# Optimization experiments

Hardware: AMD Instinct MI355X
Metric: run time of the kernel (lower is better)

## Reference

```python
import jax, jax.numpy as jnp
import numpy as np

H = 512  # hidden_size


def setup_inputs() -> dict:
    key = jax.random.key(0)
    ks = jax.random.split(key, 8)
    B, L = 16, 2048
    query = jax.random.normal(ks[0], (B, 1, 2 * H), dtype=jnp.float32)
    keys = jax.random.normal(ks[1], (B, L, 2 * H), dtype=jnp.float32)
    coverage = jax.random.uniform(ks[2], (B, L, 1), dtype=jnp.float32)
    # alignment MLP: Linear(4H+1 -> 2H, bias) -> tanh -> Linear(2H -> 1, no bias) -> softmax(dim=1)
    s1 = 1.0 / np.sqrt(4 * H + 1)
    W1 = jax.random.uniform(ks[3], (4 * H + 1, 2 * H), jnp.float32, -s1, s1)
    b1 = jax.random.uniform(ks[4], (2 * H,), jnp.float32, -s1, s1)
    s2 = 1.0 / np.sqrt(2 * H)
    W2 = jax.random.uniform(ks[5], (2 * H, 1), jnp.float32, -s2, s2)
    # reduce: Linear(2H -> H, no bias)
    Wr = jax.random.uniform(ks[6], (2 * H, H), jnp.float32, -s2, s2)
    return {"query": query, "keys": keys, "coverage": coverage,
            "W1": W1, "b1": b1, "W2": W2, "Wr": Wr}


def reference(query, keys, coverage, W1, b1, W2, Wr):
    B, L, _ = keys.shape
    q = jnp.broadcast_to(query, (B, L, query.shape[-1]))          # (B,L,2H)
    feat = jnp.concatenate([q, keys, coverage], axis=-1)          # (B,L,4H+1)
    h = jnp.tanh(feat @ W1 + b1)                                  # (B,L,2H)
    scores = h @ W2                                               # (B,L,1)
    attention = jax.nn.softmax(scores, axis=1)                    # softmax over length
    reduced = keys @ Wr                                           # (B,L,H)
    context = jnp.einsum('blo,blh->boh', attention, reduced)      # (B,1,H)
    return context, attention
```

## Files before the change

kernel.cpp:

```cpp
#include <hip/hip_runtime.h>
#include <hip/hip_bf16.h>
#include <stdint.h>

typedef short bf16x8 __attribute__((ext_vector_type(8)));
typedef float f32x4 __attribute__((ext_vector_type(4)));
typedef unsigned int u32x2 __attribute__((ext_vector_type(2)));
typedef unsigned int u32x4 __attribute__((ext_vector_type(4)));

__device__ __forceinline__ uint32_t pack2f(float lo, float hi) {
  union { __hip_bfloat162 h; uint32_t u; } c;
  c.h.x = __float2bfloat16(lo);
  c.h.y = __float2bfloat16(hi);
  return c.u;
}

__device__ __forceinline__ unsigned short f32_to_bf16(float f) {
  union { __hip_bfloat16 h; unsigned short u; } c;
  c.h = __float2bfloat16(f);
  return c.u;
}

__device__ __forceinline__ float bfbits_to_f32(uint32_t hi16) {
  union { uint32_t u; float f; } c;
  c.u = hi16 << 16;
  return c.f;
}

__device__ __forceinline__ float fast_tanh(float x) {
  float e = __builtin_amdgcn_exp2f(x * 2.8853900817779268f);
  return 1.0f - 2.0f * __builtin_amdgcn_rcpf(e + 1.0f);
}

#define GLD16(g, l)                                                                    \
  __builtin_amdgcn_global_load_lds((const __attribute__((address_space(1))) void*)(g), \
                                   (__attribute__((address_space(3))) void*)(l), 16, 0, 0)

#define MFMA16(a, b, c) __builtin_amdgcn_mfma_f32_16x16x32_bf16(a, b, c, 0, 0, 0)
#define SBAR0() __builtin_amdgcn_sched_barrier(0)

__global__ void transpose_w1k(const float* __restrict__ W1, unsigned short* __restrict__ W1kt) {
  __shared__ float t[64][65];
  const int kb = blockIdx.x * 64;
  const int jb = blockIdx.y * 64;
  const int c = threadIdx.x & 63;
  const int r = threadIdx.x >> 6;
#pragma unroll
  for (int i = 0; i < 16; ++i) {
    const int k = i * 4 + r;
    t[k][c] = W1[(size_t)(1024 + kb + k) * 1024 + (jb + c)];
  }
  __syncthreads();
#pragma unroll
  for (int i = 0; i < 16; ++i) {
    const int j = i * 4 + r;
    W1kt[(size_t)(jb + j) * 1024 + (kb + c)] = f32_to_bf16(t[c][j]);
  }
}

__global__ void convert_keys(const float* __restrict__ keys, unsigned short* __restrict__ keysbf) {
  const int bid = blockIdx.x, tid = threadIdx.x;
#pragma unroll
  for (int it = 0; it < 2; ++it) {
    const size_t c8 = ((size_t)bid * 512 + it * 256 + tid) * 8;
    f32x4 a = *(const f32x4*)(keys + c8);
    f32x4 b = *(const f32x4*)(keys + c8 + 4);
    u32x4 p;
    p.x = pack2f(a.x, a.y);
    p.y = pack2f(a.z, a.w);
    p.z = pack2f(b.x, b.y);
    p.w = pack2f(b.z, b.w);
    *(u32x4*)(keysbf + c8) = p;
  }
}

__global__ void qterm_kernel(const float* __restrict__ query, const float* __restrict__ W1,
                             const float* __restrict__ b1, float* __restrict__ qterm) {
  const int b = blockIdx.y;
  const int j = blockIdx.x * 64 + (threadIdx.x & 63);
  const int kq = threadIdx.x >> 6;
  __shared__ float part[4][64];
  const float* q = query + b * 1024 + kq * 256;
  const float* wp = W1 + (size_t)(kq * 256) * 1024 + j;
  float acc = 0.f;
#pragma unroll 8
  for (int k = 0; k < 256; ++k) acc += q[k] * wp[(size_t)k * 1024];
  part[kq][threadIdx.x & 63] = acc;
  __syncthreads();
  if (threadIdx.x < 64) {
    const int jj = blockIdx.x * 64 + threadIdx.x;
    qterm[b * 1024 + jj] = b1[jj] + part[0][threadIdx.x] + part[1][threadIdx.x] +
                           part[2][threadIdx.x] + part[3][threadIdx.x];
  }
}


#define STAGE_T(t_, src, Dd)                               \
  _Pragma("unroll") for (int i = 0; i < 4; ++i) {          \
    const int r = w * 32 + i * 8 + (lane >> 3);            \
    const int u = (lane & 7) ^ (r & 7);                    \
    GLD16((src) + (((size_t)r) << 10) + (t_) * 64 + u * 8, \
          (Dd) + w * 4096 + lane * 16 + i * 1024);         \
  }

#define V11_COMPUTE(Asrc, Bsrc)                                                          \
  _Pragma("unroll") for (int kk = 0; kk < 2; ++kk) {                                     \
    bf16x8 af[8], bfv[4];                                                                \
    _Pragma("unroll") for (int mf = 0; mf < 8; ++mf) {                                   \
      const int ra = wm * 128 + mf * 16 + c16;                                           \
      af[mf] = *(const bf16x8*)((Asrc) + ra * 128 + (((kk * 4 + q4) ^ (ra & 7)) << 4));  \
    }                                                                                    \
    _Pragma("unroll") for (int nf = 0; nf < 4; ++nf) {                                   \
      const int ca = wn * 64 + nf * 16 + c16;                                            \
      bfv[nf] = *(const bf16x8*)((Bsrc) + ca * 128 + (((kk * 4 + q4) ^ (ca & 7)) << 4)); \
    }                                                                                    \
    _Pragma("unroll") for (int nf = 0; nf < 4; ++nf)                                     \
        _Pragma("unroll") for (int mf = 0; mf < 8; ++mf) acc[mf][nf] =                   \
            MFMA16(af[mf], bfv[nf], acc[mf][nf]);                                        \
  }

#define V11_ITER(t_, Ac, Bc, An, Bn)                          \
  if ((t_) < 15) {                                            \
    STAGE_T((t_) + 1, gAbase, An);                            \
    STAGE_T((t_) + 1, gBbase, Bn);                            \
  }                                                           \
  SBAR0();                                                    \
  V11_COMPUTE(Ac, Bc);                                        \
  SBAR0();                                                    \
  asm volatile("s_waitcnt vmcnt(0) lgkmcnt(0)" ::: "memory"); \
  __builtin_amdgcn_s_barrier();

__global__ __launch_bounds__(512, 2) void gemm_score_v11(
    const unsigned short* __restrict__ keysbf, const unsigned short* __restrict__ W1kt,
    const float* __restrict__ qterm, const float* __restrict__ coverage,
    const float* __restrict__ W1, const float* __restrict__ W2,
    float* __restrict__ scores_part) {
  __shared__ __align__(16) unsigned char lds[135168];
  unsigned char* A0 = lds;
  unsigned char* A1 = lds + 32768;
  unsigned char* B0 = lds + 65536;
  unsigned char* B1 = lds + 98304;
  float* Sred = (float*)(lds + 131072);

  const int tid = threadIdx.x;
  const int bid = blockIdx.x;
  const int xcd = bid & 7;
  const int idx = bid >> 3;
  const int rowt = xcd * 16 + (idx >> 2);
  const int colgrp = idx & 3;
  const int row0 = rowt * 256;
  const int col0 = colgrp * 256;
  const int b = row0 >> 11;
  const int w = tid >> 6;
  const int wm = w >> 2, wn = w & 3;
  const int lane = tid & 63;
  const int c16 = lane & 15, q4 = lane >> 4;

  const unsigned short* gAbase = keysbf + ((size_t)row0 << 10);
  const unsigned short* gBbase = W1kt + ((size_t)col0 << 10);

  f32x4 acc[8][4];
  const f32x4 zz = {0.f, 0.f, 0.f, 0.f};
#pragma unroll
  for (int mf = 0; mf < 8; ++mf)
#pragma unroll
    for (int nf = 0; nf < 4; ++nf) acc[mf][nf] = zz;

  STAGE_T(0, gAbase, A0);
  STAGE_T(0, gBbase, B0);
  asm volatile("s_waitcnt vmcnt(0)" ::: "memory");
  __builtin_amdgcn_s_barrier();

#pragma unroll 1
  for (int th = 0; th < 8; ++th) {
    const int t0 = th * 2, t1 = th * 2 + 1;
    V11_ITER(t0, A0, B0, A1, B1);
    V11_ITER(t1, A1, B1, A0, B0);
  }

  float covv[8][4];
#pragma unroll
  for (int mf = 0; mf < 8; ++mf)
#pragma unroll
    for (int r = 0; r < 4; ++r)
      covv[mf][r] = coverage[row0 + wm * 128 + mf * 16 + q4 * 4 + r];

  float p_part[8][4];
#pragma unroll
  for (int mf = 0; mf < 8; ++mf)
#pragma unroll
    for (int r = 0; r < 4; ++r) p_part[mf][r] = 0.f;

#pragma unroll
  for (int nf = 0; nf < 4; ++nf) {
    const int col = col0 + wn * 64 + nf * 16 + c16;
    const float qt = qterm[b * 1024 + col];
    const float w1c = W1[(size_t)2048 * 1024 + col];
    const float w2 = W2[col];
#pragma unroll
    for (int mf = 0; mf < 8; ++mf)
#pragma unroll
      for (int r = 0; r < 4; ++r) {
        float v = acc[mf][nf][r] + qt + covv[mf][r] * w1c;
        p_part[mf][r] += fast_tanh(v) * w2;
      }
  }

#pragma unroll
  for (int mf = 0; mf < 8; ++mf)
#pragma unroll
    for (int r = 0; r < 4; ++r) {
      float p = p_part[mf][r];
      p += __shfl_xor(p, 1);
      p += __shfl_xor(p, 2);
      p += __shfl_xor(p, 4);
      p += __shfl_xor(p, 8);
      if (c16 == 0) Sred[w * 128 + mf * 16 + q4 * 4 + r] = p;
    }
  __syncthreads();
  if (tid < 256) {
    const int wmv = tid >> 7, rl = tid & 127;
    float s = Sred[(wmv * 4 + 0) * 128 + rl] + Sred[(wmv * 4 + 1) * 128 + rl] +
              Sred[(wmv * 4 + 2) * 128 + rl] + Sred[(wmv * 4 + 3) * 128 + rl];
    scores_part[(size_t)colgrp * 32768 + row0 + tid] = s;
  }
}

__global__ void softmax_kernel(const float* __restrict__ sp, float* __restrict__ att) {
  const int b = blockIdx.x;
  const int tid = threadIdx.x;
  float* a = att + b * 2048;
  __shared__ float red[4];
  float mx = -1e30f;
  for (int l = tid; l < 2048; l += 256) {
    float v = 0.f;
#pragma unroll
    for (int g = 0; g < 4; ++g) v += sp[(size_t)g * 32768 + b * 2048 + l];
    a[l] = v;
    mx = fmaxf(mx, v);
  }
#pragma unroll
  for (int o = 1; o < 64; o <<= 1) mx = fmaxf(mx, __shfl_xor(mx, o));
  if ((tid & 63) == 0) red[tid >> 6] = mx;
  __syncthreads();
  mx = fmaxf(fmaxf(red[0], red[1]), fmaxf(red[2], red[3]));
  __syncthreads();
  float sum = 0.f;
  for (int l = tid; l < 2048; l += 256) {
    float e = __expf(a[l] - mx);
    a[l] = e;
    sum += e;
  }
#pragma unroll
  for (int o = 1; o < 64; o <<= 1) sum += __shfl_xor(sum, o);
  if ((tid & 63) == 0) red[tid >> 6] = sum;
  __syncthreads();
  sum = red[0] + red[1] + red[2] + red[3];
  const float inv = 1.0f / sum;
  for (int l = tid; l < 2048; l += 256) a[l] *= inv;
}

__global__ void ctxpre_kernel(const unsigned short* __restrict__ keysbf,
                              const float* __restrict__ att, float* __restrict__ ctx_part) {
  const int b = blockIdx.x;
  const int sl = blockIdx.y;
  const int tid = threadIdx.x;
  const float* ab = att + b * 2048 + sl * 128;
  const unsigned short* kb = keysbf + ((size_t)b * 2048 + sl * 128) * 1024 + tid * 4;
  f32x4 acc = {0.f, 0.f, 0.f, 0.f};
#pragma unroll 4
  for (int l = 0; l < 128; ++l) {
    u32x2 v = *(const u32x2*)(kb + (size_t)l * 1024);
    const float al = ab[l];
    acc.x += bfbits_to_f32(v.x & 0xFFFFu) * al;
    acc.y += bfbits_to_f32(v.x >> 16) * al;
    acc.z += bfbits_to_f32(v.y & 0xFFFFu) * al;
    acc.w += bfbits_to_f32(v.y >> 16) * al;
  }
  *(f32x4*)(ctx_part + ((size_t)(sl * 16 + b)) * 1024 + tid * 4) = acc;
}

__global__ void ctxreduce_kernel(const float* __restrict__ ctx_part, float* __restrict__ ctx_pre) {
  const int i = blockIdx.x * 256 + threadIdx.x;
  const int b = i >> 10, j = i & 1023;
  float s = 0.f;
#pragma unroll
  for (int sl = 0; sl < 16; ++sl) s += ctx_part[((size_t)(sl * 16 + b)) * 1024 + j];
  ctx_pre[i] = s;
}

__global__ void context_kernel(const float* __restrict__ ctx_pre, const float* __restrict__ Wr,
                               float* __restrict__ out) {
  const int b = blockIdx.y;
  const int h = blockIdx.x * 64 + (threadIdx.x & 63);
  const int jq = threadIdx.x >> 6;
  __shared__ float part[4][64];
  const float* cp = ctx_pre + b * 1024 + jq * 256;
  const float* wp = Wr + (size_t)(jq * 256) * 512 + h;
  float acc = 0.f;
#pragma unroll 8
  for (int k = 0; k < 256; ++k) acc += cp[k] * wp[(size_t)k * 512];
  part[jq][threadIdx.x & 63] = acc;
  __syncthreads();
  if (threadIdx.x < 64)
    out[b * 512 + blockIdx.x * 64 + threadIdx.x] = part[0][threadIdx.x] + part[1][threadIdx.x] +
                                                   part[2][threadIdx.x] + part[3][threadIdx.x];
}

extern "C" void kernel_launch(void* const* d_in, const int* in_sizes, int n_in, void* d_out,
                              int out_size, void* d_ws, size_t ws_size, hipStream_t stream) {
  const float* query = (const float*)d_in[0];
  const float* keys = (const float*)d_in[1];
  const float* coverage = (const float*)d_in[2];
  const float* W1 = (const float*)d_in[3];
  const float* b1 = (const float*)d_in[4];
  const float* W2 = (const float*)d_in[5];
  const float* Wr = (const float*)d_in[6];
  float* out = (float*)d_out;
  char* ws = (char*)d_ws;

  float* scores_part = (float*)ws;
  float* ctx_part = (float*)ws;
  float* ctx_pre = (float*)(ws + 1048576);
  float* qterm = (float*)(ws + 1114112);
  unsigned short* W1kt = (unsigned short*)(ws + 1179648);
  unsigned short* keysbf = (unsigned short*)(ws + 3276800);

  float* context_out = out;
  float* att_out = out + 8192;

  transpose_w1k<<<dim3(16, 16), dim3(256), 0, stream>>>(W1, W1kt);
  convert_keys<<<dim3(8192), dim3(256), 0, stream>>>(keys, keysbf);
  qterm_kernel<<<dim3(16, 16), dim3(256), 0, stream>>>(query, W1, b1, qterm);
  gemm_score_v11<<<dim3(512), dim3(512), 0, stream>>>(keysbf, W1kt, qterm, coverage, W1, W2,
                                                      scores_part);
  softmax_kernel<<<dim3(16), dim3(256), 0, stream>>>(scores_part, att_out);
  ctxpre_kernel<<<dim3(16, 16), dim3(256), 0, stream>>>(keysbf, att_out, ctx_part);
  ctxreduce_kernel<<<dim3(64), dim3(256), 0, stream>>>(ctx_part, ctx_pre);
  context_kernel<<<dim3(8, 16), dim3(256), 0, stream>>>(ctx_pre, Wr, context_out);
}
```

Before: 164.0 us.

## Triple-buffer GEMM K-loop and merge prep and context kernels

Replaces the double-buffered K=64 GEMM main loop with a three-stage K=32 pipeline. It waits with a partial vmcnt so that loads stay in flight across the barrier, and raises wave priority around the MFMA block. The three preprocessing kernels (key conversion, W1 transpose, qterm) are merged into one launch, and the ctx reduce is fused into the final context projection, cutting launches. The cost is a smaller k-step, more barriers per tile, and redundant reduction of ctx_part across the 8 hb blocks.

Result: faster. 147.0 us (-10.4%).

```diff
diff --git a/kernel.cpp b/kernel.cpp
--- a/kernel.cpp
+++ b/kernel.cpp
@@ -38,108 +38,111 @@
 #define MFMA16(a, b, c) __builtin_amdgcn_mfma_f32_16x16x32_bf16(a, b, c, 0, 0, 0)
 #define SBAR0() __builtin_amdgcn_sched_barrier(0)
 
-__global__ void transpose_w1k(const float* __restrict__ W1, unsigned short* __restrict__ W1kt) {
-  __shared__ float t[64][65];
-  const int kb = blockIdx.x * 64;
-  const int jb = blockIdx.y * 64;
-  const int c = threadIdx.x & 63;
-  const int r = threadIdx.x >> 6;
-#pragma unroll
-  for (int i = 0; i < 16; ++i) {
-    const int k = i * 4 + r;
-    t[k][c] = W1[(size_t)(1024 + kb + k) * 1024 + (jb + c)];
-  }
-  __syncthreads();
-#pragma unroll
-  for (int i = 0; i < 16; ++i) {
-    const int j = i * 4 + r;
-    W1kt[(size_t)(jb + j) * 1024 + (kb + c)] = f32_to_bf16(t[c][j]);
-  }
-}
-
-__global__ void convert_keys(const float* __restrict__ keys, unsigned short* __restrict__ keysbf) {
-  const int bid = blockIdx.x, tid = threadIdx.x;
-#pragma unroll
-  for (int it = 0; it < 2; ++it) {
-    const size_t c8 = ((size_t)bid * 512 + it * 256 + tid) * 8;
-    f32x4 a = *(const f32x4*)(keys + c8);
-    f32x4 b = *(const f32x4*)(keys + c8 + 4);
-    u32x4 p;
-    p.x = pack2f(a.x, a.y);
-    p.y = pack2f(a.z, a.w);
-    p.z = pack2f(b.x, b.y);
-    p.w = pack2f(b.z, b.w);
-    *(u32x4*)(keysbf + c8) = p;
-  }
-}
-
-__global__ void qterm_kernel(const float* __restrict__ query, const float* __restrict__ W1,
-                             const float* __restrict__ b1, float* __restrict__ qterm) {
-  const int b = blockIdx.y;
-  const int j = blockIdx.x * 64 + (threadIdx.x & 63);
-  const int kq = threadIdx.x >> 6;
-  __shared__ float part[4][64];
-  const float* q = query + b * 1024 + kq * 256;
-  const float* wp = W1 + (size_t)(kq * 256) * 1024 + j;
-  float acc = 0.f;
+__global__ void prep_kernel(const float* __restrict__ keys, unsigned short* __restrict__ keysbf,
+                            const float* __restrict__ W1, unsigned short* __restrict__ W1kt,
+                            const float* __restrict__ query, const float* __restrict__ b1,
+                            float* __restrict__ qterm) {
+  __shared__ __align__(16) unsigned char smem[16896];
+  const int bid = blockIdx.x;
+  const int t = threadIdx.x;
+  if (bid < 8192) {
+#pragma unroll
+    for (int it = 0; it < 2; ++it) {
+      const size_t c8 = ((size_t)bid * 512 + it * 256 + t) * 8;
+      f32x4 a = *(const f32x4*)(keys + c8);
+      f32x4 b = *(const f32x4*)(keys + c8 + 4);
+      u32x4 p;
+      p.x = pack2f(a.x, a.y);
+      p.y = pack2f(a.z, a.w);
+      p.z = pack2f(b.x, b.y);
+      p.w = pack2f(b.z, b.w);
+      *(u32x4*)(keysbf + c8) = p;
+    }
+  } else if (bid < 8448) {
+    float (*tt)[65] = (float(*)[65])smem;
+    const int tb = bid - 8192;
+    const int kb = (tb & 15) * 64;
+    const int jb = (tb >> 4) * 64;
+    const int c = t & 63;
+    const int r = t >> 6;
+#pragma unroll
+    for (int i = 0; i < 16; ++i) {
+      const int k = i * 4 + r;
+      tt[k][c] = W1[(size_t)(1024 + kb + k) * 1024 + (jb + c)];
+    }
+    __syncthreads();
+#pragma unroll
+    for (int i = 0; i < 16; ++i) {
+      const int j = i * 4 + r;
+      W1kt[(size_t)(jb + j) * 1024 + (kb + c)] = f32_to_bf16(tt[c][j]);
+    }
+  } else {
+    float (*part)[64] = (float(*)[64])smem;
+    const int q = bid - 8448;
+    const int b = q >> 4;
+    const int j = (q & 15) * 64 + (t & 63);
+    const int kq = t >> 6;
+    const float* qp = query + b * 1024 + kq * 256;
+    const float* wp = W1 + (size_t)(kq * 256) * 1024 + j;
+    float acc = 0.f;
 #pragma unroll 8
-  for (int k = 0; k < 256; ++k) acc += q[k] * wp[(size_t)k * 1024];
-  part[kq][threadIdx.x & 63] = acc;
-  __syncthreads();
-  if (threadIdx.x < 64) {
-    const int jj = blockIdx.x * 64 + threadIdx.x;
-    qterm[b * 1024 + jj] = b1[jj] + part[0][threadIdx.x] + part[1][threadIdx.x] +
-                           part[2][threadIdx.x] + part[3][threadIdx.x];
-  }
-}
-
-
-#define STAGE_T(t_, src, Dd)                               \
-  _Pragma("unroll") for (int i = 0; i < 4; ++i) {          \
-    const int r = w * 32 + i * 8 + (lane >> 3);            \
-    const int u = (lane & 7) ^ (r & 7);                    \
-    GLD16((src) + (((size_t)r) << 10) + (t_) * 64 + u * 8, \
-          (Dd) + w * 4096 + lane * 16 + i * 1024);         \
-  }
-
-#define V11_COMPUTE(Asrc, Bsrc)                                                          \
-  _Pragma("unroll") for (int kk = 0; kk < 2; ++kk) {                                     \
-    bf16x8 af[8], bfv[4];                                                                \
-    _Pragma("unroll") for (int mf = 0; mf < 8; ++mf) {                                   \
-      const int ra = wm * 128 + mf * 16 + c16;                                           \
-      af[mf] = *(const bf16x8*)((Asrc) + ra * 128 + (((kk * 4 + q4) ^ (ra & 7)) << 4));  \
-    }                                                                                    \
-    _Pragma("unroll") for (int nf = 0; nf < 4; ++nf) {                                   \
-      const int ca = wn * 64 + nf * 16 + c16;                                            \
-      bfv[nf] = *(const bf16x8*)((Bsrc) + ca * 128 + (((kk * 4 + q4) ^ (ca & 7)) << 4)); \
-    }                                                                                    \
-    _Pragma("unroll") for (int nf = 0; nf < 4; ++nf)                                     \
-        _Pragma("unroll") for (int mf = 0; mf < 8; ++mf) acc[mf][nf] =                   \
-            MFMA16(af[mf], bfv[nf], acc[mf][nf]);                                        \
-  }
-
-#define V11_ITER(t_, Ac, Bc, An, Bn)                          \
-  if ((t_) < 15) {                                            \
-    STAGE_T((t_) + 1, gAbase, An);                            \
-    STAGE_T((t_) + 1, gBbase, Bn);                            \
-  }                                                           \
-  SBAR0();                                                    \
-  V11_COMPUTE(Ac, Bc);                                        \
-  SBAR0();                                                    \
-  asm volatile("s_waitcnt vmcnt(0) lgkmcnt(0)" ::: "memory"); \
-  __builtin_amdgcn_s_barrier();
-
-__global__ __launch_bounds__(512, 2) void gemm_score_v11(
+    for (int k = 0; k < 256; ++k) acc += qp[k] * wp[(size_t)k * 1024];
+    part[kq][t & 63] = acc;
+    __syncthreads();
+    if (t < 64) {
+      const int jj = (q & 15) * 64 + t;
+      qterm[b * 1024 + jj] = b1[jj] + part[0][t] + part[1][t] + part[2][t] + part[3][t];
+    }
+  }
+}
+
+
+#define V12_STAGE(kt_, P)                                                           \
+  _Pragma("unroll") for (int i = 0; i < 2; ++i) {                                   \
+    const int r = i * 128 + w * 16 + (lane >> 2);                                   \
+    const int u = (lane & 3) ^ ((r >> 1) & 3);                                      \
+    GLD16(keysbf + (size_t)(row0 + r) * 1024 + (kt_) * 32 + u * 8,                  \
+          (P) + i * 8192 + w * 1024 + lane * 16);                                   \
+    GLD16(W1kt + (size_t)(col0 + r) * 1024 + (kt_) * 32 + u * 8,                    \
+          (P) + 16384 + i * 8192 + w * 1024 + lane * 16);                           \
+  }
+
+#define V12_COMPUTE(P)                                                              \
+  {                                                                                 \
+    bf16x8 af[8], bfv[4];                                                           \
+    _Pragma("unroll") for (int mf = 0; mf < 8; ++mf) {                              \
+      const int ra = wm * 128 + mf * 16 + c16;                                      \
+      af[mf] = *(const bf16x8*)((P) + ra * 64 + ((q4 ^ ((ra >> 1) & 3)) << 4));     \
+    }                                                                               \
+    _Pragma("unroll") for (int nf = 0; nf < 4; ++nf) {                              \
+      const int ca = wn * 64 + nf * 16 + c16;                                       \
+      bfv[nf] =                                                                     \
+          *(const bf16x8*)((P) + 16384 + ca * 64 + ((q4 ^ ((ca >> 1) & 3)) << 4));  \
+    }                                                                               \
+    __builtin_amdgcn_s_setprio(1);                                                  \
+    _Pragma("unroll") for (int nf = 0; nf < 4; ++nf)                                \
+        _Pragma("unroll") for (int mf = 0; mf < 8; ++mf) acc[mf][nf] =              \
+            MFMA16(af[mf], bfv[nf], acc[mf][nf]);                                   \
+    __builtin_amdgcn_s_setprio(0);                                                  \
+  }
+
+#define V12_ITER(ts_, Pc, Ps)                             \
+  asm volatile("s_waitcnt vmcnt(4)" ::: "memory");        \
+  __builtin_amdgcn_s_barrier();                           \
+  SBAR0();                                                \
+  V12_STAGE(ts_, Ps);                                     \
+  V12_COMPUTE(Pc);
+
+__global__ __launch_bounds__(512, 2) void gemm_score_v12(
     const unsigned short* __restrict__ keysbf, const unsigned short* __restrict__ W1kt,
     const float* __restrict__ qterm, const float* __restrict__ coverage,
     const float* __restrict__ W1, const float* __restrict__ W2,
     float* __restrict__ scores_part) {
-  __shared__ __align__(16) unsigned char lds[135168];
-  unsigned char* A0 = lds;
-  unsigned char* A1 = lds + 32768;
-  unsigned char* B0 = lds + 65536;
-  unsigned char* B1 = lds + 98304;
-  float* Sred = (float*)(lds + 131072);
+  __shared__ __align__(16) unsigned char lds[102400];
+  unsigned char* P0 = lds;
+  unsigned char* P1 = lds + 32768;
+  unsigned char* P2 = lds + 65536;
+  float* Sred = (float*)(lds + 98304);
 
   const int tid = threadIdx.x;
   const int bid = blockIdx.x;
@@ -155,9 +158,6 @@
   const int lane = tid & 63;
   const int c16 = lane & 15, q4 = lane >> 4;
 
-  const unsigned short* gAbase = keysbf + ((size_t)row0 << 10);
-  const unsigned short* gBbase = W1kt + ((size_t)col0 << 10);
-
   f32x4 acc[8][4];
   const f32x4 zz = {0.f, 0.f, 0.f, 0.f};
 #pragma unroll
@@ -165,17 +165,23 @@
 #pragma unroll
     for (int nf = 0; nf < 4; ++nf) acc[mf][nf] = zz;
 
-  STAGE_T(0, gAbase, A0);
-  STAGE_T(0, gBbase, B0);
+  V12_STAGE(0, P0);
+  V12_STAGE(1, P1);
+
+#pragma unroll 1
+  for (int tb = 0; tb < 30; tb += 3) {
+    V12_ITER(tb + 2, P0, P2);
+    V12_ITER(tb + 3, P1, P0);
+    V12_ITER(tb + 4, P2, P1);
+  }
+  asm volatile("s_waitcnt vmcnt(4)" ::: "memory");
+  __builtin_amdgcn_s_barrier();
+  SBAR0();
+  V12_COMPUTE(P0);
   asm volatile("s_waitcnt vmcnt(0)" ::: "memory");
   __builtin_amdgcn_s_barrier();
-
-#pragma unroll 1
-  for (int th = 0; th < 8; ++th) {
-    const int t0 = th * 2, t1 = th * 2 + 1;
-    V11_ITER(t0, A0, B0, A1, B1);
-    V11_ITER(t1, A1, B1, A0, B0);
-  }
+  SBAR0();
+  V12_COMPUTE(P1);
 
   float covv[8][4];
 #pragma unroll
@@ -279,31 +285,32 @@
   *(f32x4*)(ctx_part + ((size_t)(sl * 16 + b)) * 1024 + tid * 4) = acc;
 }
 
-__global__ void ctxreduce_kernel(const float* __restrict__ ctx_part, float* __restrict__ ctx_pre) {
-  const int i = blockIdx.x * 256 + threadIdx.x;
-  const int b = i >> 10, j = i & 1023;
-  float s = 0.f;
-#pragma unroll
-  for (int sl = 0; sl < 16; ++sl) s += ctx_part[((size_t)(sl * 16 + b)) * 1024 + j];
-  ctx_pre[i] = s;
-}
-
-__global__ void context_kernel(const float* __restrict__ ctx_pre, const float* __restrict__ Wr,
-                               float* __restrict__ out) {
+__global__ void ctx2_kernel(const float* __restrict__ ctx_part, const float* __restrict__ Wr,
+                            float* __restrict__ out) {
+  __shared__ float cpre[1024];
+  __shared__ float part[4][64];
+  const int hb = blockIdx.x;
   const int b = blockIdx.y;
-  const int h = blockIdx.x * 64 + (threadIdx.x & 63);
-  const int jq = threadIdx.x >> 6;
-  __shared__ float part[4][64];
-  const float* cp = ctx_pre + b * 1024 + jq * 256;
+  const int t = threadIdx.x;
+#pragma unroll
+  for (int jj = 0; jj < 4; ++jj) {
+    const int j = jj * 256 + t;
+    float s = 0.f;
+#pragma unroll
+    for (int sl = 0; sl < 16; ++sl) s += ctx_part[((size_t)(sl * 16 + b)) * 1024 + j];
+    cpre[j] = s;
+  }
+  __syncthreads();
+  const int h = hb * 64 + (t & 63);
+  const int jq = t >> 6;
   const float* wp = Wr + (size_t)(jq * 256) * 512 + h;
   float acc = 0.f;
 #pragma unroll 8
-  for (int k = 0; k < 256; ++k) acc += cp[k] * wp[(size_t)k * 512];
-  part[jq][threadIdx.x & 63] = acc;
-  __syncthreads();
-  if (threadIdx.x < 64)
-    out[b * 512 + blockIdx.x * 64 + threadIdx.x] = part[0][threadIdx.x] + part[1][threadIdx.x] +
-                                                   part[2][threadIdx.x] + part[3][threadIdx.x];
+  for (int k = 0; k < 256; ++k) acc += cpre[jq * 256 + k] * wp[(size_t)k * 512];
+  part[jq][t & 63] = acc;
+  __syncthreads();
+  if (t < 64)
+    out[b * 512 + hb * 64 + t] = part[0][t] + part[1][t] + part[2][t] + part[3][t];
 }
 
 extern "C" void kernel_launch(void* const* d_in, const int* in_sizes, int n_in, void* d_out,
@@ -320,7 +327,6 @@
 
   float* scores_part = (float*)ws;
   float* ctx_part = (float*)ws;
-  float* ctx_pre = (float*)(ws + 1048576);
   float* qterm = (float*)(ws + 1114112);
   unsigned short* W1kt = (unsigned short*)(ws + 1179648);
   unsigned short* keysbf = (unsigned short*)(ws + 3276800);
@@ -328,13 +334,10 @@
   float* context_out = out;
   float* att_out = out + 8192;
 
-  transpose_w1k<<<dim3(16, 16), dim3(256), 0, stream>>>(W1, W1kt);
-  convert_keys<<<dim3(8192), dim3(256), 0, stream>>>(keys, keysbf);
-  qterm_kernel<<<dim3(16, 16), dim3(256), 0, stream>>>(query, W1, b1, qterm);
-  gemm_score_v11<<<dim3(512), dim3(512), 0, stream>>>(keysbf, W1kt, qterm, coverage, W1, W2,
+  prep_kernel<<<dim3(8704), dim3(256), 0, stream>>>(keys, keysbf, W1, W1kt, query, b1, qterm);
+  gemm_score_v12<<<dim3(512), dim3(512), 0, stream>>>(keysbf, W1kt, qterm, coverage, W1, W2,
                                                       scores_part);
   softmax_kernel<<<dim3(16), dim3(256), 0, stream>>>(scores_part, att_out);
   ctxpre_kernel<<<dim3(16, 16), dim3(256), 0, stream>>>(keysbf, att_out, ctx_part);
-  ctxreduce_kernel<<<dim3(64), dim3(256), 0, stream>>>(ctx_part, ctx_pre);
-  context_kernel<<<dim3(8, 16), dim3(256), 0, stream>>>(ctx_pre, Wr, context_out);
-}
+  ctx2_kernel<<<dim3(8, 16), dim3(256), 0, stream>>>(ctx_part, Wr, context_out);
+}
```
